# Kernel optimization log

Hardware: AMD Instinct MI355X
Metric: run time of the kernel (lower is better)

## Reference

```python
import jax, jax.numpy as jnp
import numpy as np

B, S, Q, C = 1, 128, 256, 256
H, DH = 8, 32
TOT = H * DH  # 256


def setup_inputs() -> dict:
    key = jax.random.key(0)
    ks = jax.random.split(key, 12)
    inp = {
        'q_x': jax.random.normal(ks[0], (B, S, Q, C), jnp.float32),
        'kv_x': jax.random.normal(ks[1], (B, S, Q, C), jnp.float32),
        'bias_mask': jax.random.normal(ks[2], (B, S, 1, 1, Q), jnp.float32),
        'bias_pair': jax.random.normal(ks[3], (B, 1, H, Q, Q), jnp.float32),
        # torch nn.Linear weights are (out_features, in_features)
        'Wq': jax.random.normal(ks[4], (TOT, C), jnp.float32) * (C ** -0.5),
        'Wk': jax.random.normal(ks[5], (TOT, C), jnp.float32) * (C ** -0.5),
        'Wv': jax.random.normal(ks[6], (TOT, C), jnp.float32) * (C ** -0.5),
        'Wg': jax.random.normal(ks[7], (TOT, C), jnp.float32) * 0.02,
        'bg': jnp.ones((TOT,), jnp.float32),   # 'gating' init: zero W, bias=1
        'Wo': jax.random.normal(ks[8], (C, TOT), jnp.float32) * 0.02,
        'bo': jnp.zeros((C,), jnp.float32),
    }
    return inp


def reference(q_x, kv_x, bias_mask, bias_pair, Wq, Wk, Wv, Wg, bg, Wo, bo):
    # QKV projections (no bias), split heads, move head dim before Q: [B,S,H,Q,DH]
    def proj(x, W):
        y = jnp.einsum('bsqc,dc->bsqd', x, W)
        return y.reshape(*y.shape[:-1], H, DH).transpose(0, 1, 3, 2, 4)

    q = proj(q_x, Wq)   # NOTE: literal source applies NO 1/sqrt(dh) scaling in naive mode
    k = proj(kv_x, Wk)
    v = proj(kv_x, Wv)

    # scores [B,S,H,Q,K] with additive biases, manual softmax
    scores = jnp.einsum('bshqd,bshkd->bshqk', q, k) + bias_mask + bias_pair
    a = jax.nn.softmax(scores, axis=-1)
    o = jnp.einsum('bshqk,bshkd->bshqd', a, v)
    o = o.transpose(0, 1, 3, 2, 4)  # [B,S,Q,H,DH]

    # gating
    g = jax.nn.sigmoid(jnp.einsum('bsqc,dc->bsqd', q_x, Wg) + bg)
    o = o * g.reshape(*g.shape[:-1], H, DH)

    # output projection
    o = o.reshape(*o.shape[:-2], TOT)
    return jnp.einsum('bsqd,cd->bsqc', o, Wo) + bo
```

## Files before the change

kernel.cpp:

```cpp
#include <hip/hip_runtime.h>


typedef unsigned short u16;
typedef unsigned int   u32;
typedef float  f32x4  __attribute__((ext_vector_type(4)));
typedef __bf16 bf16x8 __attribute__((ext_vector_type(8)));

__device__ __forceinline__ float bf2f(u16 u) {
    union { u32 i; float f; } v; v.i = ((u32)u) << 16; return v.f;
}
__device__ __forceinline__ u16 f2bf(float f) {
    __bf16 h = (__bf16)f; return __builtin_bit_cast(u16, h);
}

__device__ __forceinline__ void gld16(const u16* g, u16* l) {
    __builtin_amdgcn_global_load_lds(
        (const __attribute__((address_space(1))) u32*)g,
        (__attribute__((address_space(3))) u32*)l, 16, 0, 0);
}

__device__ __forceinline__ size_t hm(int row, int col) {
    const int s = row >> 8, q = row & 255, h = col >> 5, dh = col & 31;
    return ((size_t)((h * 128 + s) * 256 + q) << 5) + dh;
}

__device__ __forceinline__ void cvt8(const float4* src, u16* dst) {
    float4 a = src[0], b = src[1];
    u16 r[8];
    r[0] = f2bf(a.x); r[1] = f2bf(a.y); r[2] = f2bf(a.z); r[3] = f2bf(a.w);
    r[4] = f2bf(b.x); r[5] = f2bf(b.y); r[6] = f2bf(b.z); r[7] = f2bf(b.w);
    *(uint4*)dst = *(uint4*)r;
}

__global__ __launch_bounds__(256) void prep(
    const float* __restrict__ qx, const float* __restrict__ kvx,
    const float* __restrict__ Wq, const float* __restrict__ Wk,
    const float* __restrict__ Wv, const float* __restrict__ Wg,
    const float* __restrict__ Wo, const float* __restrict__ bp,
    u16* __restrict__ Xq, u16* __restrict__ Xkv, u16* __restrict__ Wball,
    float* __restrict__ bppf)
{
    const int b = blockIdx.x, t = threadIdx.x;
    if (b < 4096) {
        const int e = (b * 256 + t) * 8;
        cvt8((const float4*)(qx + e), Xq + e);
    } else if (b < 8192) {
        const int e = ((b - 4096) * 256 + t) * 8;
        cvt8((const float4*)(kvx + e), Xkv + e);
    } else if (b < 8352) {
        const int b2  = b - 8192;
        const int mat = b2 >> 5;
        const float* W = (mat == 0) ? Wq : (mat == 1) ? Wk : (mat == 2) ? Wv
                       : (mat == 3) ? Wg : Wo;
        const int off = (b2 & 31) * 2048 + t * 8;
        cvt8((const float4*)(W + off), Wball + mat * 65536 + off);
    } else {
        const int b3 = b - 8352;
        const int u0 = (b3 * 256 + t) * 2;
        #pragma unroll
        for (int k2 = 0; k2 < 2; ++k2) {
            const int u  = u0 + k2;
            const int l  = u & 63;
            const int nt = (u >> 6) & 15;
            const int tt = u >> 10;
            const int ww = tt & 3, qqt = (tt >> 2) & 3, hh = tt >> 4;
            const int q  = qqt * 64 + ww * 16 + (l & 15);
            const int kp = nt * 16 + (l >> 4) * 4;
            const float4 v = *(const float4*)(bp + (size_t)(hh * 256 + q) * 256 + kp);
            *(float4*)(bppf + (size_t)u * 4) = v;
        }
    }
}

__global__ __launch_bounds__(256) void proj_all(
    const u16* __restrict__ Xq, const u16* __restrict__ Xkv,
    const u16* __restrict__ Wball, const float* __restrict__ bg,
    u16* __restrict__ Qh, u16* __restrict__ Kh, u16* __restrict__ Vh, u16* __restrict__ Gh)
{
    __shared__ u16 At[128 * 64];
    __shared__ u16 Wt[128 * 64];

    const int bid = blockIdx.x;
    const int mb  = bid & 255;
    const int nb  = bid >> 8;
    const int t   = nb >> 1;
    const int n0  = (nb & 1) * 128;
    const int m0  = mb * 128;
    const u16* A = (t == 0 || t == 3) ? Xq : Xkv;
    const u16* W = Wball + t * 65536;
    u16*       O = (t == 0) ? Qh : (t == 1) ? Kh : (t == 2) ? Vh : Gh;

    const int tid  = threadIdx.x;
    const int lane = tid & 63;
    const int w    = tid >> 6;
    const int quad = lane >> 4;
    const int ln   = lane & 15;
    const int wm   = (w >> 1) * 64;
    const int wn   = (w & 1) * 64;
    const int lrow = lane >> 3;
    const int lcol = (lane & 7) * 8;

    f32x4 acc[4][4] = {};

    for (int k0 = 0; k0 < 256; k0 += 64) {
        __syncthreads();
        #pragma unroll
        for (int qq = 0; qq < 4; ++qq) {
            const int r = w * 32 + qq * 8;
            gld16(A + (size_t)(m0 + r + lrow) * 256 + k0 + lcol, &At[r * 64]);
            gld16(W + (size_t)(n0 + r + lrow) * 256 + k0 + lcol, &Wt[r * 64]);
        }
        __syncthreads();

        #pragma unroll
        for (int kk = 0; kk < 2; ++kk) {
            const int kc = kk * 32 + quad * 8;
            bf16x8 af[4], bfr[4];
            #pragma unroll
            for (int i = 0; i < 4; ++i)
                af[i] = __builtin_bit_cast(bf16x8, *(const uint4*)&At[(wm + i * 16 + ln) * 64 + kc]);
            #pragma unroll
            for (int j = 0; j < 4; ++j)
                bfr[j] = __builtin_bit_cast(bf16x8, *(const uint4*)&Wt[(wn + j * 16 + ln) * 64 + kc]);
            #pragma unroll
            for (int i = 0; i < 4; ++i)
                #pragma unroll
                for (int j = 0; j < 4; ++j)
                    acc[i][j] = __builtin_amdgcn_mfma_f32_16x16x32_bf16(bfr[j], af[i], acc[i][j], 0, 0, 0);
        }
    }

    const int act = (t == 3);
    #pragma unroll
    for (int i = 0; i < 4; ++i) {
        const int row = m0 + wm + i * 16 + ln;
        #pragma unroll
        for (int j = 0; j < 4; ++j) {
            const int colb = n0 + wn + j * 16 + quad * 4;
            u16 r4[4];
            if (act) {
                const float4 bgv = *(const float4*)&bg[colb];
                float v0 = acc[i][j][0] + bgv.x;
                float v1 = acc[i][j][1] + bgv.y;
                float v2 = acc[i][j][2] + bgv.z;
                float v3 = acc[i][j][3] + bgv.w;
                r4[0] = f2bf(1.0f / (1.0f + __expf(-v0)));
                r4[1] = f2bf(1.0f / (1.0f + __expf(-v1)));
                r4[2] = f2bf(1.0f / (1.0f + __expf(-v2)));
                r4[3] = f2bf(1.0f / (1.0f + __expf(-v3)));
            } else {
                r4[0] = f2bf(acc[i][j][0]);
                r4[1] = f2bf(acc[i][j][1]);
                r4[2] = f2bf(acc[i][j][2]);
                r4[3] = f2bf(acc[i][j][3]);
            }
            *(uint2*)(O + hm(row, colb)) = *(const uint2*)r4;
        }
    }
}

__global__ __launch_bounds__(256) void gemm_out(
    const u16* __restrict__ Oh, const u16* __restrict__ Wob,
    const float* __restrict__ bo, float* __restrict__ out)
{
    __shared__ u16 At[64 * 64];
    __shared__ u16 Wt[128 * 64];

    const int bid = blockIdx.x;
    const int m0  = (bid & 511) * 64;
    const int n0  = (bid >> 9) * 128;

    const int tid  = threadIdx.x;
    const int lane = tid & 63;
    const int w    = tid >> 6;
    const int quad = lane >> 4;
    const int ln   = lane & 15;
    const int wm   = (w >> 1) * 32;
    const int wn   = (w & 1) * 64;
    const int lrow = lane >> 3;
    const int lcol = (lane & 7) * 8;

    f32x4 acc[2][4] = {};

    for (int k0 = 0; k0 < 256; k0 += 64) {
        __syncthreads();
        #pragma unroll
        for (int qq = 0; qq < 2; ++qq) {
            const int r = w * 16 + qq * 8;
            gld16(Oh + hm(m0 + r + lrow, k0 + lcol), &At[r * 64]);
        }
        #pragma unroll
        for (int qq = 0; qq < 4; ++qq) {
            const int r = w * 32 + qq * 8;
            gld16(Wob + (size_t)(n0 + r + lrow) * 256 + k0 + lcol, &Wt[r * 64]);
        }
        __syncthreads();

        #pragma unroll
        for (int kk = 0; kk < 2; ++kk) {
            const int kc = kk * 32 + quad * 8;
            bf16x8 af[2], bfr[4];
            #pragma unroll
            for (int i = 0; i < 2; ++i)
                af[i] = __builtin_bit_cast(bf16x8, *(const uint4*)&At[(wm + i * 16 + ln) * 64 + kc]);
            #pragma unroll
            for (int j = 0; j < 4; ++j)
                bfr[j] = __builtin_bit_cast(bf16x8, *(const uint4*)&Wt[(wn + j * 16 + ln) * 64 + kc]);
            #pragma unroll
            for (int i = 0; i < 2; ++i)
                #pragma unroll
                for (int j = 0; j < 4; ++j)
                    acc[i][j] = __builtin_amdgcn_mfma_f32_16x16x32_bf16(bfr[j], af[i], acc[i][j], 0, 0, 0);
        }
    }

    #pragma unroll
    for (int i = 0; i < 2; ++i) {
        const int row = m0 + wm + i * 16 + ln;
        #pragma unroll
        for (int j = 0; j < 4; ++j) {
            const int colb = n0 + wn + j * 16 + quad * 4;
            const float4 bov = *(const float4*)&bo[colb];
            float4 o;
            o.x = acc[i][j][0] + bov.x;
            o.y = acc[i][j][1] + bov.y;
            o.z = acc[i][j][2] + bov.z;
            o.w = acc[i][j][3] + bov.w;
            *(float4*)&out[(size_t)row * 256 + colb] = o;
        }
    }
}

__global__ __launch_bounds__(256, 2) void attn_kernel(
    const u16* __restrict__ Qh, const u16* __restrict__ Kh, const u16* __restrict__ Vh,
    const u16* __restrict__ Gh, const float* __restrict__ bm, const float* __restrict__ bppf,
    u16* __restrict__ Oh)
{
    __shared__ u16   Vt[32][264];
    __shared__ u16   Pl[4][16][76];
    __shared__ float bmf[256];

    const int hs   = blockIdx.x;
    const int h    = hs & 7;
    const int s    = hs >> 3;
    const int tid  = threadIdx.x;
    const int lane = tid & 63;
    const int w    = tid >> 6;
    const int quad = lane >> 4;
    const int ln   = lane & 15;

    const size_t hsBase = ((size_t)(h * 128 + s) * 256) << 5;

    {
        const uint4* vp = (const uint4*)(Vh + hsBase + (size_t)tid * 32);
        uint4 vv0 = vp[0], vv1 = vp[1], vv2 = vp[2], vv3 = vp[3];
        u16 tmp[32];
        *(uint4*)&tmp[0]  = vv0; *(uint4*)&tmp[8]  = vv1;
        *(uint4*)&tmp[16] = vv2; *(uint4*)&tmp[24] = vv3;
        #pragma unroll
        for (int dh = 0; dh < 32; ++dh) Vt[dh][tid] = tmp[dh];
        bmf[tid] = bm[s * 256 + tid];
    }
    __syncthreads();

    for (int iq = 0; iq < 2; ++iq) {
        const int qt = blockIdx.y * 2 + iq;
        const int q0 = qt * 64 + w * 16;

        bf16x8 aq = __builtin_bit_cast(bf16x8,
            *(const uint4*)(Qh + hsBase + (size_t)(q0 + ln) * 32 + quad * 8));

        const float* bpt = bppf + ((size_t)(((h * 4 + qt) * 4 + w) * 16) * 64 + lane) * 4;

        f32x4 sc[16];
        float rmax[4] = {-1e30f, -1e30f, -1e30f, -1e30f};
        #pragma unroll
        for (int c = 0; c < 4; ++c) {
            bf16x8 bk[4];
            f32x4  bv[4];
            #pragma unroll
            for (int j = 0; j < 4; ++j) {
                const int nt = c * 4 + j;
                bk[j] = __builtin_bit_cast(bf16x8,
                    *(const uint4*)(Kh + hsBase + (size_t)(nt * 16 + ln) * 32 + quad * 8));
                bv[j] = *(const f32x4*)(bpt + (size_t)nt * 256);
            }
            #pragma unroll
            for (int j = 0; j < 4; ++j) {
                const int nt = c * 4 + j;
                f32x4 z = {0.f, 0.f, 0.f, 0.f};
                f32x4 r = __builtin_amdgcn_mfma_f32_16x16x32_bf16(bk[j], aq, z, 0, 0, 0);
                const f32x4 bm4 = *(const f32x4*)&bmf[nt * 16 + quad * 4];
                #pragma unroll
                for (int rr = 0; rr < 4; ++rr) {
                    float v = r[rr] + bm4[rr] + bv[j][rr];
                    sc[nt][rr] = v;
                    rmax[rr] = fmaxf(rmax[rr], v);
                }
            }
            __builtin_amdgcn_sched_barrier(0);
        }

        float m = fmaxf(fmaxf(rmax[0], rmax[1]), fmaxf(rmax[2], rmax[3]));
        m = fmaxf(m, __shfl_xor(m, 16));
        m = fmaxf(m, __shfl_xor(m, 32));

        float s4[4] = {0.f, 0.f, 0.f, 0.f};
        #pragma unroll
        for (int nt = 0; nt < 16; ++nt)
            #pragma unroll
            for (int rr = 0; rr < 4; ++rr) {
                float p = __expf(sc[nt][rr] - m);
                sc[nt][rr] = p;
                s4[rr] += p;
            }
        float tsum = (s4[0] + s4[1]) + (s4[2] + s4[3]);
        tsum += __shfl_xor(tsum, 16);
        tsum += __shfl_xor(tsum, 32);
        const float rinv = 1.0f / tsum;

        f32x4 o0 = {0.f, 0.f, 0.f, 0.f}, o1 = {0.f, 0.f, 0.f, 0.f};
        #pragma unroll
        for (int c = 0; c < 4; ++c) {
            #pragma unroll
            for (int ntl = 0; ntl < 4; ++ntl) {
                const int nt = c * 4 + ntl;
                u16 r4[4];
                #pragma unroll
                for (int rr = 0; rr < 4; ++rr)
                    r4[rr] = f2bf(sc[nt][rr] * rinv);
                *(uint2*)&Pl[w][ln][ntl * 16 + quad * 4] = *(const uint2*)r4;
            }
            #pragma unroll
            for (int kcl = 0; kcl < 2; ++kcl) {
                bf16x8 pa = __builtin_bit_cast(bf16x8, *(const uint4*)&Pl[w][ln][kcl * 32 + quad * 8]);
                bf16x8 v0 = __builtin_bit_cast(bf16x8, *(const uint4*)&Vt[ln][c * 64 + kcl * 32 + quad * 8]);
                bf16x8 v1 = __builtin_bit_cast(bf16x8, *(const uint4*)&Vt[16 + ln][c * 64 + kcl * 32 + quad * 8]);
                o0 = __builtin_amdgcn_mfma_f32_16x16x32_bf16(v0, pa, o0, 0, 0, 0);
                o1 = __builtin_amdgcn_mfma_f32_16x16x32_bf16(v1, pa, o1, 0, 0, 0);
            }
        }

        const size_t base = hsBase + (size_t)(q0 + ln) * 32;
        const uint2 ga = *(const uint2*)(Gh + base + quad * 4);
        const uint2 gb = *(const uint2*)(Gh + base + 16 + quad * 4);
        const u16* gau = (const u16*)&ga;
        const u16* gbu = (const u16*)&gb;
        u16 ra[4], rb[4];
        #pragma unroll
        for (int rr = 0; rr < 4; ++rr) {
            ra[rr] = f2bf(o0[rr] * bf2f(gau[rr]));
            rb[rr] = f2bf(o1[rr] * bf2f(gbu[rr]));
        }
        *(uint2*)(Oh + base + quad * 4)      = *(const uint2*)ra;
        *(uint2*)(Oh + base + 16 + quad * 4) = *(const uint2*)rb;
    }
}

extern "C" void kernel_launch(void* const* d_in, const int* in_sizes, int n_in,
                              void* d_out, int out_size, void* d_ws, size_t ws_size,
                              hipStream_t stream)
{
    const float* qx  = (const float*)d_in[0];
    const float* kvx = (const float*)d_in[1];
    const float* bm  = (const float*)d_in[2];
    const float* bp  = (const float*)d_in[3];
    const float* Wq  = (const float*)d_in[4];
    const float* Wk  = (const float*)d_in[5];
    const float* Wv  = (const float*)d_in[6];
    const float* Wg  = (const float*)d_in[7];
    const float* bg  = (const float*)d_in[8];
    const float* Wo  = (const float*)d_in[9];
    const float* bo  = (const float*)d_in[10];
    float* out = (float*)d_out;

    const size_t NEL = (size_t)32768 * 256;
    u16* Qh = (u16*)d_ws;
    u16* Kh = Qh + NEL;
    u16* Vh = Kh + NEL;
    u16* Gh = Vh + NEL;
    u16* Wball = Gh + NEL;
    float* bppf = (float*)(Wball + 5 * 65536);

    u16* Xq  = (u16*)d_out;
    u16* Xkv = Xq + NEL;

    prep<<<dim3(8608), dim3(256), 0, stream>>>(qx, kvx, Wq, Wk, Wv, Wg, Wo, bp,
                                               Xq, Xkv, Wball, bppf);

    proj_all<<<dim3(2048), dim3(256), 0, stream>>>(Xq, Xkv, Wball, bg, Qh, Kh, Vh, Gh);

    attn_kernel<<<dim3(1024, 2), dim3(256), 0, stream>>>(Qh, Kh, Vh, Gh, bm, bppf, Qh );

    gemm_out<<<dim3(1024), dim3(256), 0, stream>>>(Qh , Wball + 4 * 65536, bo, out);
}
```

Measured before the change: 213.5 us.

## Fuse fp32-to-bf16 input conversion into projection GEMM and merge attention query tiles

```diff
diff --git a/kernel.cpp b/kernel.cpp
--- a/kernel.cpp
+++ b/kernel.cpp
@@ -33,29 +33,20 @@
 }
 
 __global__ __launch_bounds__(256) void prep(
-    const float* __restrict__ qx, const float* __restrict__ kvx,
     const float* __restrict__ Wq, const float* __restrict__ Wk,
     const float* __restrict__ Wv, const float* __restrict__ Wg,
     const float* __restrict__ Wo, const float* __restrict__ bp,
-    u16* __restrict__ Xq, u16* __restrict__ Xkv, u16* __restrict__ Wball,
-    float* __restrict__ bppf)
+    u16* __restrict__ Wball, float* __restrict__ bppf)
 {
     const int b = blockIdx.x, t = threadIdx.x;
-    if (b < 4096) {
-        const int e = (b * 256 + t) * 8;
-        cvt8((const float4*)(qx + e), Xq + e);
-    } else if (b < 8192) {
-        const int e = ((b - 4096) * 256 + t) * 8;
-        cvt8((const float4*)(kvx + e), Xkv + e);
-    } else if (b < 8352) {
-        const int b2  = b - 8192;
-        const int mat = b2 >> 5;
+    if (b < 160) {
+        const int mat = b >> 5;
         const float* W = (mat == 0) ? Wq : (mat == 1) ? Wk : (mat == 2) ? Wv
                        : (mat == 3) ? Wg : Wo;
-        const int off = (b2 & 31) * 2048 + t * 8;
+        const int off = (b & 31) * 2048 + t * 8;
         cvt8((const float4*)(W + off), Wball + mat * 65536 + off);
     } else {
-        const int b3 = b - 8352;
+        const int b3 = b - 160;
         const int u0 = (b3 * 256 + t) * 2;
         #pragma unroll
         for (int k2 = 0; k2 < 2; ++k2) {
@@ -73,7 +64,7 @@
 }
 
 __global__ __launch_bounds__(256) void proj_all(
-    const u16* __restrict__ Xq, const u16* __restrict__ Xkv,
+    const float* __restrict__ Xqf, const float* __restrict__ Xkvf,
     const u16* __restrict__ Wball, const float* __restrict__ bg,
     u16* __restrict__ Qh, u16* __restrict__ Kh, u16* __restrict__ Vh, u16* __restrict__ Gh)
 {
@@ -86,7 +77,7 @@
     const int t   = nb >> 1;
     const int n0  = (nb & 1) * 128;
     const int m0  = mb * 128;
-    const u16* A = (t == 0 || t == 3) ? Xq : Xkv;
+    const float* Af = (t == 0 || t == 3) ? Xqf : Xkvf;
     const u16* W = Wball + t * 65536;
     u16*       O = (t == 0) ? Qh : (t == 1) ? Kh : (t == 2) ? Vh : Gh;
 
@@ -107,8 +98,13 @@
         #pragma unroll
         for (int qq = 0; qq < 4; ++qq) {
             const int r = w * 32 + qq * 8;
-            gld16(A + (size_t)(m0 + r + lrow) * 256 + k0 + lcol, &At[r * 64]);
             gld16(W + (size_t)(n0 + r + lrow) * 256 + k0 + lcol, &Wt[r * 64]);
+        }
+        #pragma unroll
+        for (int qq = 0; qq < 4; ++qq) {
+            const int r = w * 32 + qq * 8 + lrow;
+            cvt8((const float4*)(Af + (size_t)(m0 + r) * 256 + k0 + lcol),
+                 &At[r * 64 + lcol]);
         }
         __syncthreads();
 
@@ -263,12 +259,16 @@
     }
     __syncthreads();
 
-    for (int iq = 0; iq < 2; ++iq) {
-        const int qt = blockIdx.y * 2 + iq;
+    for (int iq = 0; iq < 4; ++iq) {
+        const int qt = iq;
         const int q0 = qt * 64 + w * 16;
 
         bf16x8 aq = __builtin_bit_cast(bf16x8,
             *(const uint4*)(Qh + hsBase + (size_t)(q0 + ln) * 32 + quad * 8));
+
+        const size_t obase = hsBase + (size_t)(q0 + ln) * 32;
+        const uint2 ga = *(const uint2*)(Gh + obase + quad * 4);
+        const uint2 gb = *(const uint2*)(Gh + obase + 16 + quad * 4);
 
         const float* bpt = bppf + ((size_t)(((h * 4 + qt) * 4 + w) * 16) * 64 + lane) * 4;
 
@@ -341,9 +341,6 @@
             }
         }
 
-        const size_t base = hsBase + (size_t)(q0 + ln) * 32;
-        const uint2 ga = *(const uint2*)(Gh + base + quad * 4);
-        const uint2 gb = *(const uint2*)(Gh + base + 16 + quad * 4);
         const u16* gau = (const u16*)&ga;
         const u16* gbu = (const u16*)&gb;
         u16 ra[4], rb[4];
@@ -352,8 +349,8 @@
             ra[rr] = f2bf(o0[rr] * bf2f(gau[rr]));
             rb[rr] = f2bf(o1[rr] * bf2f(gbu[rr]));
         }
-        *(uint2*)(Oh + base + quad * 4)      = *(const uint2*)ra;
-        *(uint2*)(Oh + base + 16 + quad * 4) = *(const uint2*)rb;
+        *(uint2*)(Oh + obase + quad * 4)      = *(const uint2*)ra;
+        *(uint2*)(Oh + obase + 16 + quad * 4) = *(const uint2*)rb;
     }
 }
 
@@ -382,15 +379,11 @@
     u16* Wball = Gh + NEL;
     float* bppf = (float*)(Wball + 5 * 65536);
 
-    u16* Xq  = (u16*)d_out;
-    u16* Xkv = Xq + NEL;
-
-    prep<<<dim3(8608), dim3(256), 0, stream>>>(qx, kvx, Wq, Wk, Wv, Wg, Wo, bp,
-                                               Xq, Xkv, Wball, bppf);
-
-    proj_all<<<dim3(2048), dim3(256), 0, stream>>>(Xq, Xkv, Wball, bg, Qh, Kh, Vh, Gh);
-
-    attn_kernel<<<dim3(1024, 2), dim3(256), 0, stream>>>(Qh, Kh, Vh, Gh, bm, bppf, Qh );
+    prep<<<dim3(416), dim3(256), 0, stream>>>(Wq, Wk, Wv, Wg, Wo, bp, Wball, bppf);
+
+    proj_all<<<dim3(2048), dim3(256), 0, stream>>>(qx, kvx, Wball, bg, Qh, Kh, Vh, Gh);
+
+    attn_kernel<<<dim3(1024), dim3(256), 0, stream>>>(Qh, Kh, Vh, Gh, bm, bppf, Qh );
 
     gemm_out<<<dim3(1024), dim3(256), 0, stream>>>(Qh , Wball + 4 * 65536, bo, out);
 }
```

New measurement: 212.2 us. Within noise of the previous version (-0.6%).
